# Optimization experiments

Measured on AMD Instinct MI355X. Metric: run time of the kernel, lower is better.

Reference implementation:

```python
import jax, jax.numpy as jnp
import numpy as np

N = 20000      # atoms
E = 320000     # edges
F = 128        # node_size (hard-pinned by split(128) / expand to 384)
RBF = 20
RC = 5.0
ITERS = 3
NM = 64        # molecules in batch


def setup_inputs() -> dict:
    key = jax.random.key(0)
    ks = iter(jax.random.split(key, 64))
    def nrm(shape, scale=0.05):
        return jax.random.normal(next(ks), shape, dtype=jnp.float32) * scale
    inp = {}
    inp["z"] = jax.random.randint(next(ks), (N,), 0, 119)
    inp["graph"] = jax.random.randint(next(ks), (E, 2), 0, N)
    inp["edges_dist"] = jax.random.uniform(next(ks), (E,), minval=0.5, maxval=RC, dtype=jnp.float32)
    sense = jax.random.normal(next(ks), (E, 3), dtype=jnp.float32)
    inp["edges_sense"] = sense / jnp.linalg.norm(sense, axis=1, keepdims=True)
    inp["graph_idx"] = jnp.sort(jax.random.randint(next(ks), (N,), 0, NM))
    # parameters (stacked over ITERS message/update blocks)
    inp["emb"] = nrm((119, F), 1.0)
    inp["mw1"] = nrm((ITERS, F, F)); inp["mb1"] = nrm((ITERS, F))
    inp["mw2"] = nrm((ITERS, 3 * F, F)); inp["mb2"] = nrm((ITERS, 3 * F))
    inp["ew"] = nrm((ITERS, 3 * F, RBF)); inp["eb"] = nrm((ITERS, 3 * F))
    inp["uw"] = nrm((ITERS, F, F)); inp["vw"] = nrm((ITERS, F, F))
    inp["aw1"] = nrm((ITERS, F, 2 * F)); inp["ab1"] = nrm((ITERS, F))
    inp["aw2"] = nrm((ITERS, 3 * F, F)); inp["ab2"] = nrm((ITERS, 3 * F))
    inp["ow1"] = nrm((F, F)); inp["ob1"] = nrm((F,))
    inp["ow2"] = nrm((1, F)); inp["ob2"] = nrm((1,))
    return inp


def reference(z, graph, edges_dist, edges_sense, graph_idx,
              emb, mw1, mb1, mw2, mb2, ew, eb,
              uw, vw, aw1, ab1, aw2, ab2, ow1, ob1, ow2, ob2):
    src = graph[:, 0]   # scatter target (index_add index)
    dst = graph[:, 1]   # gather source (neighbour)
    s = emb[z]                                  # [N, F]
    v = jnp.zeros((N, 3, F), dtype=s.dtype)     # [N, 3, F]
    # edge-level precompute (same every iteration)
    n = jnp.arange(1, RBF + 1, dtype=jnp.float32)
    d = edges_dist[:, None]
    rbf = jnp.sin(n * jnp.pi * d / RC) / d                              # [E, RBF]
    cut = 0.5 * (jnp.cos(jnp.pi * edges_dist / RC) + 1.0) * (edges_dist < RC)  # [E]
    for i in range(ITERS):
        # --- Message block ---
        a = jax.nn.silu(s @ mw1[i].T + mb1[i]) @ mw2[i].T + mb2[i]      # [N, 3F]
        dist_rep = (rbf @ ew[i].T + eb[i]) * cut[:, None]               # [E, 3F]
        res = a[dst] * dist_rep                                         # [E, 3F]
        rv, rs, rd = res[:, :F], res[:, F:2 * F], res[:, 2 * F:]
        resv = v[dst] * rv[:, None, :] + edges_sense[:, :, None] * rd[:, None, :]  # [E,3,F]
        s = s + 2.0 * jax.ops.segment_sum(rs, src, num_segments=N)
        v = v + 2.0 * jax.ops.segment_sum(resv, src, num_segments=N)
        # --- Update block ---
        Uv = v @ uw[i].T                                                # [N,3,F]
        Vv = v @ vw[i].T
        h = jnp.concatenate([s, jnp.linalg.norm(Vv, axis=1)], axis=-1)  # [N, 2F]
        a2 = jax.nn.silu(h @ aw1[i].T + ab1[i]) @ aw2[i].T + ab2[i]     # [N, 3F]
        avv, asv, ass = a2[:, :F], a2[:, F:2 * F], a2[:, 2 * F:]
        s = s + ass + asv * jnp.sum(Uv * Vv, axis=1)
        v = v + avv[:, None, :] * Uv
    out = jax.nn.silu(s @ ow1.T + ob1) @ ow2.T + ob2                    # [N, 1]
    return jax.ops.segment_sum(out, graph_idx, num_segments=NM)         # [NM, 1]
```

## Files before the change

### kernel.cpp

```cpp
#include <hip/hip_runtime.h>
#include <math.h>

#define NN 20000
#define NE 320000
#define FD 128
#define RBFN 20
#define RC_ 5.0f
#define NITER 3
#define NMOL 64
#define F3 384
#define F2 256
#define PI_ 3.14159265358979323846f
#define KB 128
#define LPAD 8

typedef __attribute__((ext_vector_type(8))) short  bf16x8;
typedef __attribute__((ext_vector_type(4))) float  floatx4;
typedef unsigned short u16;

__device__ __forceinline__ u16 f2b(float x) {
    union { float f; unsigned int u; } v; v.f = x;
    unsigned int u = v.u;
    return (u16)((u + 0x7fffu + ((u >> 16) & 1u)) >> 16);
}
__device__ __forceinline__ float b2f(u16 x) {
    union { unsigned int u; float f; } v; v.u = ((unsigned int)x) << 16;
    return v.f;
}

__global__ __launch_bounds__(256) void cvt_w_kernel(
    const float* s0, int n0, const float* s1, int n1, const float* s2, int n2,
    const float* s3, int n3, const float* s4, int n4, const float* s5, int n5,
    const float* s6, int n6, u16* __restrict__ dst)
{
    int idx = blockIdx.x * 256 + threadIdx.x;
    if (idx < n0) { dst[idx] = f2b(s0[idx]); return; } idx -= n0; dst += n0;
    if (idx < n1) { dst[idx] = f2b(s1[idx]); return; } idx -= n1; dst += n1;
    if (idx < n2) { dst[idx] = f2b(s2[idx]); return; } idx -= n2; dst += n2;
    if (idx < n3) { dst[idx] = f2b(s3[idx]); return; } idx -= n3; dst += n3;
    if (idx < n4) { dst[idx] = f2b(s4[idx]); return; } idx -= n4; dst += n4;
    if (idx < n5) { dst[idx] = f2b(s5[idx]); return; } idx -= n5; dst += n5;
    if (idx < n6) { dst[idx] = f2b(s6[idx]); }
}

__global__ __launch_bounds__(256) void cvt_ew_kernel(const float* __restrict__ ew,
    u16* __restrict__ ewb)
{
    int idx = blockIdx.x * 256 + threadIdx.x;
    if (idx >= NITER * F3 * 32) return;
    int k = idx & 31;
    int row = idx >> 5;
    ewb[idx] = (k < RBFN) ? f2b(ew[row * RBFN + k]) : (u16)0;
}

__global__ __launch_bounds__(256) void embed_kernel(const int* __restrict__ z,
    const float* __restrict__ emb, float* __restrict__ s, u16* __restrict__ sbf)
{
    int idx = blockIdx.x * 256 + threadIdx.x;
    if (idx >= NN * FD) return;
    int n = idx >> 7, f = idx & 127;
    float v = emb[z[n] * FD + f];
    s[idx] = v; sbf[idx] = f2b(v);
}

__global__ __launch_bounds__(256) void zero_f_kernel(float* __restrict__ p, int n)
{
    int idx = blockIdx.x * 256 + threadIdx.x;
    if (idx < n) p[idx] = 0.f;
}

__global__ __launch_bounds__(256) void zero_i_kernel(int* __restrict__ p, int n)
{
    int idx = blockIdx.x * 256 + threadIdx.x;
    if (idx < n) p[idx] = 0;
}

__global__ __launch_bounds__(256) void csr_count_kernel(const int* __restrict__ graph,
    int* __restrict__ cnt)
{
    int e = blockIdx.x * 256 + threadIdx.x;
    if (e >= NE) return;
    atomicAdd(&cnt[graph[2 * e]], 1);
}

__global__ __launch_bounds__(1024) void csr_scan_kernel(const int* __restrict__ cnt,
    int* __restrict__ row_ptr, int* __restrict__ cursor)
{
    __shared__ int sd[1024];
    int tid = threadIdx.x;
    const int chunk = (NN + 1023) / 1024;
    int start = tid * chunk;
    int end = start + chunk; if (end > NN) end = NN;
    int sum = 0;
    for (int j = start; j < end; j++) sum += cnt[j];
    sd[tid] = sum;
    __syncthreads();
    for (int off = 1; off < 1024; off <<= 1) {
        int v = 0;
        if (tid >= off) v = sd[tid - off];
        __syncthreads();
        if (tid >= off) sd[tid] += v;
        __syncthreads();
    }
    int run = (tid == 0) ? 0 : sd[tid - 1];
    for (int j = start; j < end; j++) {
        row_ptr[j] = run;
        cursor[j]  = run;
        run += cnt[j];
    }
    if (tid == 0) row_ptr[NN] = NE;
}

__global__ __launch_bounds__(256) void csr_scatter_kernel(const int* __restrict__ graph,
    int* __restrict__ cursor, int* __restrict__ edge_list)
{
    int e = blockIdx.x * 256 + threadIdx.x;
    if (e >= NE) return;
    int p = atomicAdd(&cursor[graph[2 * e]], 1);
    edge_list[p] = e;
}

__global__ __launch_bounds__(256) void edge_stream_kernel(
    const int* __restrict__ edge_list, const int* __restrict__ graph,
    const float* __restrict__ dist, const float* __restrict__ sense,
    u16* __restrict__ rbf_bf, float* __restrict__ cut_p,
    float* __restrict__ sense_p, int* __restrict__ dst_p)
{
    int j = blockIdx.x * 256 + threadIdx.x;
    if (j >= NE) return;
    int e = edge_list[j];
    float d = dist[e];
    float inv = 1.f / d;
    float base = PI_ * d / RC_;
    u16* rb = rbf_bf + (size_t)j * 32;
    #pragma unroll
    for (int k = 0; k < RBFN; k++)
        rb[k] = f2b(sinf((float)(k + 1) * base) * inv);
    #pragma unroll
    for (int k = RBFN; k < 32; k++) rb[k] = 0;
    cut_p[j] = 0.5f * (cosf(base) + 1.f) * (d < RC_ ? 1.f : 0.f);
    dst_p[j] = graph[2 * e + 1];
    sense_p[3 * j + 0] = sense[3 * e + 0];
    sense_p[3 * j + 1] = sense[3 * e + 1];
    sense_p[3 * j + 2] = sense[3 * e + 2];
}

template<bool SILU>
__global__ __launch_bounds__(256) void gemm_bf16(const u16* __restrict__ A,
    const u16* __restrict__ Wt, const float* __restrict__ bias,
    float* __restrict__ C, u16* __restrict__ Cb, int M, int K, int Nc)
{
    __shared__ u16 As[64][KB + LPAD];
    __shared__ u16 Bs[64][KB + LPAD];
    const int bm = blockIdx.x * 64;
    const int bn = blockIdx.y * 64;
    const int tid = threadIdx.x;
    const int r = tid >> 2;
    const int q = tid & 3;
    const int wave = tid >> 6;
    const int lane = tid & 63;
    const int wm = (wave >> 1) * 32;
    const int wn = (wave & 1) * 32;
    const int quad = lane >> 4;
    const int lr = lane & 15;

    floatx4 acc[2][2];
    #pragma unroll
    for (int i = 0; i < 2; i++)
        #pragma unroll
        for (int j = 0; j < 2; j++)
            acc[i][j] = (floatx4)0.f;

    for (int ko = 0; ko < K; ko += KB) {
        {
            int gm = bm + r;
            u16* dA = &As[r][q * 32];
            if (gm < M) {
                const u16* ap = A + (size_t)gm * K + ko + q * 32;
                #pragma unroll
                for (int x = 0; x < 32; x += 8)
                    *(bf16x8*)&dA[x] = *(const bf16x8*)(ap + x);
            } else {
                #pragma unroll
                for (int x = 0; x < 32; x += 8)
                    *(bf16x8*)&dA[x] = (bf16x8)0;
            }
        }
        {
            int gn = bn + r;
            const u16* wp = Wt + (size_t)gn * K + ko + q * 32;
            u16* dB = &Bs[r][q * 32];
            #pragma unroll
            for (int x = 0; x < 32; x += 8)
                *(bf16x8*)&dB[x] = *(const bf16x8*)(wp + x);
        }
        __syncthreads();
        #pragma unroll
        for (int kk = 0; kk < KB; kk += 32) {
            bf16x8 a0 = *(const bf16x8*)&As[wm + lr     ][kk + quad * 8];
            bf16x8 a1 = *(const bf16x8*)&As[wm + 16 + lr][kk + quad * 8];
            bf16x8 b0 = *(const bf16x8*)&Bs[wn + lr     ][kk + quad * 8];
            bf16x8 b1 = *(const bf16x8*)&Bs[wn + 16 + lr][kk + quad * 8];
            acc[0][0] = __builtin_amdgcn_mfma_f32_16x16x32_bf16(a0, b0, acc[0][0], 0, 0, 0);
            acc[0][1] = __builtin_amdgcn_mfma_f32_16x16x32_bf16(a0, b1, acc[0][1], 0, 0, 0);
            acc[1][0] = __builtin_amdgcn_mfma_f32_16x16x32_bf16(a1, b0, acc[1][0], 0, 0, 0);
            acc[1][1] = __builtin_amdgcn_mfma_f32_16x16x32_bf16(a1, b1, acc[1][1], 0, 0, 0);
        }
        __syncthreads();
    }

    #pragma unroll
    for (int i = 0; i < 2; i++) {
        #pragma unroll
        for (int j = 0; j < 2; j++) {
            int gn = bn + wn + j * 16 + lr;
            float bb = bias ? bias[gn] : 0.f;
            #pragma unroll
            for (int rr = 0; rr < 4; rr++) {
                int gm = bm + wm + i * 16 + quad * 4 + rr;
                if (gm < M) {
                    float v = acc[i][j][rr] + bb;
                    if (SILU) v = v / (1.f + __expf(-v));
                    if (C)  C [(size_t)gm * Nc + gn] = v;
                    if (Cb) Cb[(size_t)gm * Nc + gn] = f2b(v);
                }
            }
        }
    }
}

template<int K1>
__global__ __launch_bounds__(256) void mlp_kernel(const u16* __restrict__ A,
    const u16* __restrict__ W1, const float* __restrict__ b1,
    const u16* __restrict__ W2, const float* __restrict__ b2,
    u16* __restrict__ Ob, int M)
{
    __shared__ u16 As[64][KB + LPAD];
    __shared__ u16 Ws[128][KB + LPAD];
    __shared__ u16 T[64][KB + LPAD];
    const int bm = blockIdx.x * 64;
    const int tid = threadIdx.x;
    const int wave = tid >> 6, lane = tid & 63;
    const int wm  = (wave >> 1) * 32;
    const int wn1 = (wave & 1) * 64;
    const int wn  = (wave & 1) * 32;
    const int quad = lane >> 4, lr = lane & 15;
    const int r = tid >> 2, q = tid & 3;

    floatx4 acc1[2][4];
    #pragma unroll
    for (int i = 0; i < 2; i++)
        #pragma unroll
        for (int j = 0; j < 4; j++) acc1[i][j] = (floatx4)0.f;

    for (int ko = 0; ko < K1; ko += KB) {
        {
            int gm = bm + r;
            u16* dA = &As[r][q * 32];
            if (gm < M) {
                const u16* ap = A + (size_t)gm * K1 + ko + q * 32;
                #pragma unroll
                for (int x = 0; x < 32; x += 8)
                    *(bf16x8*)&dA[x] = *(const bf16x8*)(ap + x);
            } else {
                #pragma unroll
                for (int x = 0; x < 32; x += 8)
                    *(bf16x8*)&dA[x] = (bf16x8)0;
            }
            #pragma unroll
            for (int h = 0; h < 2; h++) {
                int wr = r + h * 64;
                const u16* wp = W1 + (size_t)wr * K1 + ko + q * 32;
                u16* dW = &Ws[wr][q * 32];
                #pragma unroll
                for (int x = 0; x < 32; x += 8)
                    *(bf16x8*)&dW[x] = *(const bf16x8*)(wp + x);
            }
        }
        __syncthreads();
        #pragma unroll
        for (int kk = 0; kk < KB; kk += 32) {
            bf16x8 a0 = *(const bf16x8*)&As[wm + lr     ][kk + quad * 8];
            bf16x8 a1 = *(const bf16x8*)&As[wm + 16 + lr][kk + quad * 8];
            #pragma unroll
            for (int j = 0; j < 4; j++) {
                bf16x8 b = *(const bf16x8*)&Ws[wn1 + j * 16 + lr][kk + quad * 8];
                acc1[0][j] = __builtin_amdgcn_mfma_f32_16x16x32_bf16(a0, b, acc1[0][j], 0, 0, 0);
                acc1[1][j] = __builtin_amdgcn_mfma_f32_16x16x32_bf16(a1, b, acc1[1][j], 0, 0, 0);
            }
        }
        __syncthreads();
    }
    #pragma unroll
    for (int i = 0; i < 2; i++) {
        #pragma unroll
        for (int j = 0; j < 4; j++) {
            int col = wn1 + j * 16 + lr;
            float bb = b1[col];
            #pragma unroll
            for (int rr = 0; rr < 4; rr++) {
                int row = wm + i * 16 + quad * 4 + rr;
                float v = acc1[i][j][rr] + bb;
                v = v / (1.f + __expf(-v));
                T[row][col] = f2b(v);
            }
        }
    }
    __syncthreads();

    for (int c0 = 0; c0 < F3; c0 += 64) {
        {
            const u16* wp = W2 + (size_t)(c0 + r) * KB + q * 32;
            u16* dW = &Ws[r][q * 32];
            #pragma unroll
            for (int x = 0; x < 32; x += 8)
                *(bf16x8*)&dW[x] = *(const bf16x8*)(wp + x);
        }
        __syncthreads();
        floatx4 acc2[2][2];
        #pragma unroll
        for (int i = 0; i < 2; i++)
            #pragma unroll
            for (int j = 0; j < 2; j++) acc2[i][j] = (floatx4)0.f;
        #pragma unroll
        for (int kk = 0; kk < KB; kk += 32) {
            bf16x8 a0 = *(const bf16x8*)&T[wm + lr     ][kk + quad * 8];
            bf16x8 a1 = *(const bf16x8*)&T[wm + 16 + lr][kk + quad * 8];
            bf16x8 b0 = *(const bf16x8*)&Ws[wn + lr     ][kk + quad * 8];
            bf16x8 b1 = *(const bf16x8*)&Ws[wn + 16 + lr][kk + quad * 8];
            acc2[0][0] = __builtin_amdgcn_mfma_f32_16x16x32_bf16(a0, b0, acc2[0][0], 0, 0, 0);
            acc2[0][1] = __builtin_amdgcn_mfma_f32_16x16x32_bf16(a0, b1, acc2[0][1], 0, 0, 0);
            acc2[1][0] = __builtin_amdgcn_mfma_f32_16x16x32_bf16(a1, b0, acc2[1][0], 0, 0, 0);
            acc2[1][1] = __builtin_amdgcn_mfma_f32_16x16x32_bf16(a1, b1, acc2[1][1], 0, 0, 0);
        }
        #pragma unroll
        for (int i = 0; i < 2; i++) {
            #pragma unroll
            for (int j = 0; j < 2; j++) {
                int gn = c0 + wn + j * 16 + lr;
                float bb = b2[gn];
                #pragma unroll
                for (int rr = 0; rr < 4; rr++) {
                    int gm = bm + wm + i * 16 + quad * 4 + rr;
                    if (gm < M)
                        Ob[(size_t)gm * F3 + gn] = f2b(acc2[i][j][rr] + bb);
                }
            }
        }
        __syncthreads();
    }
}

__global__ __launch_bounds__(256) void gemm_uv(const u16* __restrict__ A,
    const u16* __restrict__ Wu, const u16* __restrict__ Wv,
    u16* __restrict__ U, u16* __restrict__ V, int M)
{
    __shared__ u16 As[64][KB + LPAD];
    __shared__ u16 Bu[64][KB + LPAD];
    __shared__ u16 Bv[64][KB + LPAD];
    const int bm = blockIdx.x * 64;
    const int bn = blockIdx.y * 64;
    const int tid = threadIdx.x;
    const int r = tid >> 2;
    const int q = tid & 3;
    const int wave = tid >> 6;
    const int lane = tid & 63;
    const int wm = (wave >> 1) * 32;
    const int wn = (wave & 1) * 32;
    const int quad = lane >> 4;
    const int lr = lane & 15;

    floatx4 au[2][2], av[2][2];
    #pragma unroll
    for (int i = 0; i < 2; i++)
        #pragma unroll
        for (int j = 0; j < 2; j++) { au[i][j] = (floatx4)0.f; av[i][j] = (floatx4)0.f; }

    {
        int gm = bm + r;
        u16* dA = &As[r][q * 32];
        if (gm < M) {
            const u16* ap = A + (size_t)gm * KB + q * 32;
            #pragma unroll
            for (int x = 0; x < 32; x += 8)
                *(bf16x8*)&dA[x] = *(const bf16x8*)(ap + x);
        } else {
            #pragma unroll
            for (int x = 0; x < 32; x += 8)
                *(bf16x8*)&dA[x] = (bf16x8)0;
        }
        int gn = bn + r;
        const u16* up = Wu + (size_t)gn * KB + q * 32;
        const u16* vp = Wv + (size_t)gn * KB + q * 32;
        u16* dU = &Bu[r][q * 32];
        u16* dV = &Bv[r][q * 32];
        #pragma unroll
        for (int x = 0; x < 32; x += 8) {
            *(bf16x8*)&dU[x] = *(const bf16x8*)(up + x);
            *(bf16x8*)&dV[x] = *(const bf16x8*)(vp + x);
        }
    }
    __syncthreads();
    #pragma unroll
    for (int kk = 0; kk < KB; kk += 32) {
        bf16x8 a0 = *(const bf16x8*)&As[wm + lr     ][kk + quad * 8];
        bf16x8 a1 = *(const bf16x8*)&As[wm + 16 + lr][kk + quad * 8];
        bf16x8 u0 = *(const bf16x8*)&Bu[wn + lr     ][kk + quad * 8];
        bf16x8 u1 = *(const bf16x8*)&Bu[wn + 16 + lr][kk + quad * 8];
        bf16x8 v0 = *(const bf16x8*)&Bv[wn + lr     ][kk + quad * 8];
        bf16x8 v1 = *(const bf16x8*)&Bv[wn + 16 + lr][kk + quad * 8];
        au[0][0] = __builtin_amdgcn_mfma_f32_16x16x32_bf16(a0, u0, au[0][0], 0, 0, 0);
        au[0][1] = __builtin_amdgcn_mfma_f32_16x16x32_bf16(a0, u1, au[0][1], 0, 0, 0);
        au[1][0] = __builtin_amdgcn_mfma_f32_16x16x32_bf16(a1, u0, au[1][0], 0, 0, 0);
        au[1][1] = __builtin_amdgcn_mfma_f32_16x16x32_bf16(a1, u1, au[1][1], 0, 0, 0);
        av[0][0] = __builtin_amdgcn_mfma_f32_16x16x32_bf16(a0, v0, av[0][0], 0, 0, 0);
        av[0][1] = __builtin_amdgcn_mfma_f32_16x16x32_bf16(a0, v1, av[0][1], 0, 0, 0);
        av[1][0] = __builtin_amdgcn_mfma_f32_16x16x32_bf16(a1, v0, av[1][0], 0, 0, 0);
        av[1][1] = __builtin_amdgcn_mfma_f32_16x16x32_bf16(a1, v1, av[1][1], 0, 0, 0);
    }
    #pragma unroll
    for (int i = 0; i < 2; i++) {
        #pragma unroll
        for (int j = 0; j < 2; j++) {
            int gn = bn + wn + j * 16 + lr;
            #pragma unroll
            for (int rr = 0; rr < 4; rr++) {
                int gm = bm + wm + i * 16 + quad * 4 + rr;
                if (gm < M) {
                    U[(size_t)gm * FD + gn] = f2b(au[i][j][rr]);
                    V[(size_t)gm * FD + gn] = f2b(av[i][j][rr]);
                }
            }
        }
    }
}

__global__ __launch_bounds__(256) void edge_mfma_kernel(
    const u16* __restrict__ rbf_bf, const float* __restrict__ cut_p,
    const float* __restrict__ sense_p, const int* __restrict__ dst_p,
    const u16* __restrict__ ewb, const float* __restrict__ eb,
    const u16* __restrict__ a_bf, const float* __restrict__ s_in,
    const float* __restrict__ v_in, const u16* __restrict__ v_bf,
    const int* __restrict__ row_ptr,
    float* __restrict__ s_out, u16* __restrict__ s_obf,
    float* __restrict__ v_out, u16* __restrict__ v_obf)
{
    __shared__ float sdrep[16][F3 + 4];
    __shared__ float scut[16];
    __shared__ float ssen[48];
    __shared__ int   sdst[16];
    __shared__ float red[4 * 128];

    const int n = blockIdx.x;
    const int tid = threadIdx.x;
    const int wave = tid >> 6;
    const int lane = tid & 63;
    const int quad = lane >> 4;
    const int lr = lane & 15;
    const int f = tid & 127;
    const int half = tid >> 7;

    int beg = row_ptr[n], end = row_ptr[n + 1];
    float accs = 0.f, accv0 = 0.f, accv1 = 0.f, accv2 = 0.f;

    for (int t0 = beg; t0 < end; t0 += 16) {
        int cnt = end - t0; if (cnt > 16) cnt = 16;
        __syncthreads();
        if (tid < 16) {
            scut[tid] = (tid < cnt) ? cut_p[t0 + tid] : 0.f;
            sdst[tid] = (tid < cnt) ? dst_p[t0 + tid] : 0;
        }
        if (tid >= 64 && tid < 64 + 3 * cnt) ssen[tid - 64] = sense_p[3 * t0 + (tid - 64)];
        bf16x8 afrag;
        int ge = t0 + lr;
        if (ge < end) afrag = *(const bf16x8*)&rbf_bf[(size_t)ge * 32 + quad * 8];
        else          afrag = (bf16x8)0;
        floatx4 dacc[6];
        #pragma unroll
        for (int nt = 0; nt < 6; nt++) {
            int nrow = (wave * 6 + nt) * 16 + lr;
            bf16x8 bfrag = *(const bf16x8*)&ewb[(size_t)nrow * 32 + quad * 8];
            dacc[nt] = __builtin_amdgcn_mfma_f32_16x16x32_bf16(afrag, bfrag, (floatx4)0.f, 0, 0, 0);
        }
        __syncthreads();
        #pragma unroll
        for (int nt = 0; nt < 6; nt++) {
            int ncol = (wave * 6 + nt) * 16 + lr;
            float ebn = eb[ncol];
            #pragma unroll
            for (int rr = 0; rr < 4; rr++) {
                int e = quad * 4 + rr;
                sdrep[e][ncol] = (dacc[nt][rr] + ebn) * scut[e];
            }
        }
        __syncthreads();
        int e0 = half * 8;
        int e1 = e0 + 8; if (e1 > cnt) e1 = cnt;
        for (int e = e0; e < e1; e++) {
            int dst = sdst[e];
            float drv = sdrep[e][f];
            float drs = sdrep[e][FD + f];
            float drd = sdrep[e][2 * FD + f];
            const u16* ar = a_bf + (size_t)dst * F3;
            float rv = b2f(ar[f])          * drv;
            float rs = b2f(ar[FD + f])     * drs;
            float rd = b2f(ar[2 * FD + f]) * drd;
            accs += rs;
            const u16* vr = v_bf + (size_t)dst * F3;
            float sx = ssen[3 * e], sy = ssen[3 * e + 1], sz = ssen[3 * e + 2];
            accv0 += b2f(vr[f])          * rv + sx * rd;
            accv1 += b2f(vr[FD + f])     * rv + sy * rd;
            accv2 += b2f(vr[2 * FD + f]) * rv + sz * rd;
        }
    }
    __syncthreads();
    if (half == 1) {
        red[f] = accs; red[128 + f] = accv0; red[256 + f] = accv1; red[384 + f] = accv2;
    }
    __syncthreads();
    if (half == 0) {
        accs  += red[f];       accv0 += red[128 + f];
        accv1 += red[256 + f]; accv2 += red[384 + f];
        int nb = n * FD + f;
        float so = s_in[nb] + 2.f * accs;
        s_out[nb] = so; s_obf[nb] = f2b(so);
        int vb = n * F3 + f;
        float w0 = v_in[vb]           + 2.f * accv0;
        float w1 = v_in[vb + FD]      + 2.f * accv1;
        float w2 = v_in[vb + 2 * FD]  + 2.f * accv2;
        v_out[vb]          = w0; v_obf[vb]          = f2b(w0);
        v_out[vb + FD]     = w1; v_obf[vb + FD]     = f2b(w1);
        v_out[vb + 2 * FD] = w2; v_obf[vb + 2 * FD] = f2b(w2);
    }
}

__global__ __launch_bounds__(256) void build_h_kernel(const u16* __restrict__ sbf,
    const u16* __restrict__ Vv, u16* __restrict__ h)
{
    int idx = blockIdx.x * 256 + threadIdx.x;
    if (idx >= NN * FD) return;
    int n = idx >> 7, f = idx & 127;
    h[n * F2 + f] = sbf[idx];
    float x0 = b2f(Vv[n * F3 + f]);
    float x1 = b2f(Vv[n * F3 + FD + f]);
    float x2 = b2f(Vv[n * F3 + 2 * FD + f]);
    h[n * F2 + FD + f] = f2b(sqrtf(x0 * x0 + x1 * x1 + x2 * x2));
}

__global__ __launch_bounds__(256) void update_kernel(const float* __restrict__ s_mid,
    const float* __restrict__ v_mid, const u16* __restrict__ a2,
    const u16* __restrict__ Uv, const u16* __restrict__ Vv,
    float* __restrict__ s_out, u16* __restrict__ s_obf,
    float* __restrict__ v_out, u16* __restrict__ v_obf)
{
    int idx = blockIdx.x * 256 + threadIdx.x;
    if (idx >= NN * FD) return;
    int n = idx >> 7, f = idx & 127;
    int vb = n * F3 + f;
    float u0 = b2f(Uv[vb]), u1 = b2f(Uv[vb + FD]), u2 = b2f(Uv[vb + 2 * FD]);
    float w0 = b2f(Vv[vb]), w1 = b2f(Vv[vb + FD]), w2 = b2f(Vv[vb + 2 * FD]);
    float dot = u0 * w0 + u1 * w1 + u2 * w2;
    float avv = b2f(a2[n * F3 + f]);
    float asv = b2f(a2[n * F3 + FD + f]);
    float ass = b2f(a2[n * F3 + 2 * FD + f]);
    float so = s_mid[idx] + ass + asv * dot;
    s_out[idx] = so; s_obf[idx] = f2b(so);
    float y0 = v_mid[vb]          + avv * u0;
    float y1 = v_mid[vb + FD]     + avv * u1;
    float y2 = v_mid[vb + 2 * FD] + avv * u2;
    v_out[vb]          = y0; v_obf[vb]          = f2b(y0);
    v_out[vb + FD]     = y1; v_obf[vb + FD]     = f2b(y1);
    v_out[vb + 2 * FD] = y2; v_obf[vb + 2 * FD] = f2b(y2);
}

__global__ __launch_bounds__(256) void node_out_kernel(const float* __restrict__ t,
    const float* __restrict__ ow2, const float* __restrict__ ob2,
    float* __restrict__ nodeval)
{
    int gt = blockIdx.x * 256 + threadIdx.x;
    int n = gt >> 6;
    int lane = threadIdx.x & 63;
    if (n >= NN) return;
    float v = t[n * FD + lane] * ow2[lane] + t[n * FD + 64 + lane] * ow2[64 + lane];
    #pragma unroll
    for (int off = 32; off > 0; off >>= 1) v += __shfl_down(v, off);
    if (lane == 0) nodeval[n] = v + ob2[0];
}

__global__ __launch_bounds__(1024) void mol_reduce_kernel(const float* __restrict__ nodeval,
    const int* __restrict__ gidx, float* __restrict__ out)
{
    __shared__ float mol[NMOL];
    int tid = threadIdx.x;
    if (tid < NMOL) mol[tid] = 0.f;
    __syncthreads();
    int cur = -1; float acc = 0.f;
    for (int x = tid; x < NN; x += 1024) {
        int g = gidx[x];
        float v = nodeval[x];
        if (g != cur) {
            if (cur >= 0) atomicAdd(&mol[cur], acc);
            cur = g; acc = v;
        } else acc += v;
    }
    if (cur >= 0) atomicAdd(&mol[cur], acc);
    __syncthreads();
    if (tid < NMOL) out[tid] = mol[tid];
}

extern "C" void kernel_launch(void* const* d_in, const int* in_sizes, int n_in,
                              void* d_out, int out_size, void* d_ws, size_t ws_size,
                              hipStream_t stream)
{
    const int*   z     = (const int*)d_in[0];
    const int*   graph = (const int*)d_in[1];
    const float* dist  = (const float*)d_in[2];
    const float* sense = (const float*)d_in[3];
    const int*   gidx  = (const int*)d_in[4];
    const float* emb   = (const float*)d_in[5];
    const float* mw1   = (const float*)d_in[6];
    const float* mb1   = (const float*)d_in[7];
    const float* mw2   = (const float*)d_in[8];
    const float* mb2   = (const float*)d_in[9];
    const float* ew    = (const float*)d_in[10];
    const float* eb    = (const float*)d_in[11];
    const float* uw    = (const float*)d_in[12];
    const float* vw    = (const float*)d_in[13];
    const float* aw1   = (const float*)d_in[14];
    const float* ab1   = (const float*)d_in[15];
    const float* aw2   = (const float*)d_in[16];
    const float* ab2   = (const float*)d_in[17];
    const float* ow1   = (const float*)d_in[18];
    const float* ob1   = (const float*)d_in[19];
    const float* ow2   = (const float*)d_in[20];
    const float* ob2   = (const float*)d_in[21];
    float* out = (float*)d_out;

    float* W = (float*)d_ws;
    float* s_a    = W; W += (size_t)NN * FD;
    float* s_b    = W; W += (size_t)NN * FD;
    float* v_a    = W; W += (size_t)NN * F3;
    float* v_b    = W; W += (size_t)NN * F3;
    float* cut_p  = W; W += (size_t)NE;
    float* sns_p  = W; W += (size_t)NE * 3;
    float* tfin   = W; W += (size_t)NN * FD;
    float* nodeval= W; W += (size_t)NN;
    u16* U = (u16*)W;
    u16* sbf_a = U; U += (size_t)NN * FD;
    u16* sbf_b = U; U += (size_t)NN * FD;
    u16* vbf_a = U; U += (size_t)NN * F3;
    u16* vbf_b = U; U += (size_t)NN * F3;
    u16* a_bf  = U; U += (size_t)NN * F3;
    u16* a2_bf = U; U += (size_t)NN * F3;
    u16* Uv_bf = U; U += (size_t)NN * F3;
    u16* Vv_bf = U; U += (size_t)NN * F3;
    u16* rbf_bf= U; U += (size_t)NE * 32;
    u16* ewb   = U; U += (size_t)NITER * F3 * 32;
    u16* wb    = U; U += 557056;
    int* ip = (int*)U;
    int* row_ptr   = ip; ip += NN + 1;
    int* cnt       = ip; ip += NN;
    int* cursor    = ip; ip += NN;
    int* edge_list = ip; ip += NE;
    int* dst_p     = ip; ip += NE;
    u16* h_bf = a_bf;

    u16* wb_mw1 = wb;
    u16* wb_mw2 = wb + 49152;
    u16* wb_uw  = wb + 196608;
    u16* wb_vw  = wb + 245760;
    u16* wb_aw1 = wb + 294912;
    u16* wb_aw2 = wb + 393216;
    u16* wb_ow1 = wb + 540672;
    const int WTOT = 557056;

    const int TB = 256;
    dim3 b256(TB);

    cvt_w_kernel<<<dim3((WTOT + TB - 1) / TB), b256, 0, stream>>>(
        mw1, 49152, mw2, 147456, uw, 49152, vw, 49152, aw1, 98304, aw2, 147456,
        ow1, 16384, wb);
    cvt_ew_kernel<<<dim3((NITER * F3 * 32 + TB - 1) / TB), b256, 0, stream>>>(ew, ewb);
    embed_kernel<<<dim3((NN * FD + TB - 1) / TB), b256, 0, stream>>>(z, emb, s_a, sbf_a);
    zero_f_kernel<<<dim3((NN * F3 + TB - 1) / TB), b256, 0, stream>>>(v_a, NN * F3);
    zero_i_kernel<<<dim3((NN * F3 / 2 + TB - 1) / TB), b256, 0, stream>>>((int*)vbf_a, NN * F3 / 2);
    zero_i_kernel<<<dim3((NN + TB - 1) / TB), b256, 0, stream>>>(cnt, NN);
    csr_count_kernel<<<dim3((NE + TB - 1) / TB), b256, 0, stream>>>(graph, cnt);
    csr_scan_kernel<<<dim3(1), dim3(1024), 0, stream>>>(cnt, row_ptr, cursor);
    csr_scatter_kernel<<<dim3((NE + TB - 1) / TB), b256, 0, stream>>>(graph, cursor, edge_list);
    edge_stream_kernel<<<dim3((NE + TB - 1) / TB), b256, 0, stream>>>(
        edge_list, graph, dist, sense, rbf_bf, cut_p, sns_p, dst_p);

    dim3 gM((NN + 63) / 64);
    dim3 gN2((NN + 63) / 64, FD / 64);
    dim3 gV2((3 * NN + 63) / 64, FD / 64);

    for (int i = 0; i < NITER; i++) {
        mlp_kernel<128><<<gM, b256, 0, stream>>>(sbf_a,
            wb_mw1 + (size_t)i * FD * FD, mb1 + (size_t)i * FD,
            wb_mw2 + (size_t)i * F3 * FD, mb2 + (size_t)i * F3, a_bf, NN);
        edge_mfma_kernel<<<dim3(NN), b256, 0, stream>>>(
            rbf_bf, cut_p, sns_p, dst_p,
            ewb + (size_t)i * F3 * 32, eb + (size_t)i * F3,
            a_bf, s_a, v_a, vbf_a, row_ptr, s_b, sbf_b, v_b, vbf_b);
        gemm_uv<<<gV2, b256, 0, stream>>>(vbf_b, wb_uw + (size_t)i * FD * FD,
            wb_vw + (size_t)i * FD * FD, Uv_bf, Vv_bf, 3 * NN);
        build_h_kernel<<<dim3((NN * FD + TB - 1) / TB), b256, 0, stream>>>(sbf_b, Vv_bf, h_bf);
        mlp_kernel<256><<<gM, b256, 0, stream>>>(h_bf,
            wb_aw1 + (size_t)i * FD * F2, ab1 + (size_t)i * FD,
            wb_aw2 + (size_t)i * F3 * FD, ab2 + (size_t)i * F3, a2_bf, NN);
        update_kernel<<<dim3((NN * FD + TB - 1) / TB), b256, 0, stream>>>(
            s_b, v_b, a2_bf, Uv_bf, Vv_bf, s_a, sbf_a, v_a, vbf_a);
    }

    gemm_bf16<true><<<gN2, b256, 0, stream>>>(sbf_a, wb_ow1, ob1, tfin, nullptr, NN, FD, FD);
    node_out_kernel<<<dim3((NN * 64 + TB - 1) / TB), b256, 0, stream>>>(tfin, ow2, ob2, nodeval);
    mol_reduce_kernel<<<dim3(1), dim3(1024), 0, stream>>>(nodeval, gidx, out);
}
```

Before: 971.3 us.

## Pack gathered node features per channel for coalesced 8-byte edge gathers

The message MLP output and the bf16 copy of v are now written in a packed [node][feature][4] layout, so the edge kernel fetches the three channel values of a neighbour with one ushort4 load instead of three strided scalar loads. The per-edge distance representation in shared memory is also stored as packed bf16 in the same interleaved layout. The aim is fewer gather transactions and less LDS traffic in the dominant edge kernel. In exchange the gathered buffers grow by a third because of the padding lane, and storing the distance representation in bf16 instead of fp32 lowers its precision.

Result: slower. 996.8 us (+2.6%).

```diff
diff --git a/kernel.cpp b/kernel.cpp
--- a/kernel.cpp
+++ b/kernel.cpp
@@ -13,6 +13,7 @@
 #define PI_ 3.14159265358979323846f
 #define KB 128
 #define LPAD 8
+#define SD_STRIDE 516
 
 typedef __attribute__((ext_vector_type(8))) short  bf16x8;
 typedef __attribute__((ext_vector_type(4))) float  floatx4;
@@ -148,7 +149,7 @@
 template<bool SILU>
 __global__ __launch_bounds__(256) void gemm_bf16(const u16* __restrict__ A,
     const u16* __restrict__ Wt, const float* __restrict__ bias,
-    float* __restrict__ C, u16* __restrict__ Cb, int M, int K, int Nc)
+    float* __restrict__ C, int M, int K, int Nc)
 {
     __shared__ u16 As[64][KB + LPAD];
     __shared__ u16 Bs[64][KB + LPAD];
@@ -221,15 +222,14 @@
                 if (gm < M) {
                     float v = acc[i][j][rr] + bb;
                     if (SILU) v = v / (1.f + __expf(-v));
-                    if (C)  C [(size_t)gm * Nc + gn] = v;
-                    if (Cb) Cb[(size_t)gm * Nc + gn] = f2b(v);
+                    C[(size_t)gm * Nc + gn] = v;
                 }
             }
         }
     }
 }
 
-template<int K1>
+template<int K1, bool PACK>
 __global__ __launch_bounds__(256) void mlp_kernel(const u16* __restrict__ A,
     const u16* __restrict__ W1, const float* __restrict__ b1,
     const u16* __restrict__ W2, const float* __restrict__ b2,
@@ -342,8 +342,13 @@
                 #pragma unroll
                 for (int rr = 0; rr < 4; rr++) {
                     int gm = bm + wm + i * 16 + quad * 4 + rr;
-                    if (gm < M)
-                        Ob[(size_t)gm * F3 + gn] = f2b(acc2[i][j][rr] + bb);
+                    if (gm < M) {
+                        u16 val = f2b(acc2[i][j][rr] + bb);
+                        if (PACK)
+                            Ob[(size_t)gm * 512 + (gn & 127) * 4 + (gn >> 7)] = val;
+                        else
+                            Ob[(size_t)gm * F3 + gn] = val;
+                    }
                 }
             }
         }
@@ -439,15 +444,15 @@
     const u16* __restrict__ rbf_bf, const float* __restrict__ cut_p,
     const float* __restrict__ sense_p, const int* __restrict__ dst_p,
     const u16* __restrict__ ewb, const float* __restrict__ eb,
-    const u16* __restrict__ a_bf, const float* __restrict__ s_in,
-    const float* __restrict__ v_in, const u16* __restrict__ v_bf,
+    const u16* __restrict__ a_pk, const float* __restrict__ s_in,
+    const float* __restrict__ v_in, const u16* __restrict__ v_pk,
     const int* __restrict__ row_ptr,
     float* __restrict__ s_out, u16* __restrict__ s_obf,
     float* __restrict__ v_out, u16* __restrict__ v_obf)
 {
-    __shared__ float sdrep[16][F3 + 4];
+    __shared__ u16   sdrep[16 * SD_STRIDE];
     __shared__ float scut[16];
-    __shared__ float ssen[48];
+    __shared__ float ssen[16][4];
     __shared__ int   sdst[16];
     __shared__ float red[4 * 128];
 
@@ -470,7 +475,10 @@
             scut[tid] = (tid < cnt) ? cut_p[t0 + tid] : 0.f;
             sdst[tid] = (tid < cnt) ? dst_p[t0 + tid] : 0;
         }
-        if (tid >= 64 && tid < 64 + 3 * cnt) ssen[tid - 64] = sense_p[3 * t0 + (tid - 64)];
+        if (tid >= 64 && tid < 64 + 3 * cnt) {
+            int x = tid - 64;
+            ssen[x / 3][x % 3] = sense_p[3 * t0 + x];
+        }
         bf16x8 afrag;
         int ge = t0 + lr;
         if (ge < end) afrag = *(const bf16x8*)&rbf_bf[(size_t)ge * 32 + quad * 8];
@@ -486,31 +494,30 @@
         #pragma unroll
         for (int nt = 0; nt < 6; nt++) {
             int ncol = (wave * 6 + nt) * 16 + lr;
+            int fc = ncol & 127, c = ncol >> 7;
             float ebn = eb[ncol];
             #pragma unroll
             for (int rr = 0; rr < 4; rr++) {
                 int e = quad * 4 + rr;
-                sdrep[e][ncol] = (dacc[nt][rr] + ebn) * scut[e];
-            }
-        }
-        __syncthreads();
-        int e0 = half * 8;
-        int e1 = e0 + 8; if (e1 > cnt) e1 = cnt;
-        for (int e = e0; e < e1; e++) {
+                sdrep[e * SD_STRIDE + fc * 4 + c] = f2b((dacc[nt][rr] + ebn) * scut[e]);
+            }
+        }
+        __syncthreads();
+        int nh = cnt - half * 8; if (nh > 8) nh = 8;
+        for (int k = 0; k < nh; k++) {
+            int e = half * 8 + k;
             int dst = sdst[e];
-            float drv = sdrep[e][f];
-            float drs = sdrep[e][FD + f];
-            float drd = sdrep[e][2 * FD + f];
-            const u16* ar = a_bf + (size_t)dst * F3;
-            float rv = b2f(ar[f])          * drv;
-            float rs = b2f(ar[FD + f])     * drs;
-            float rd = b2f(ar[2 * FD + f]) * drd;
+            ushort4 dr = *(const ushort4*)&sdrep[e * SD_STRIDE + f * 4];
+            float drv = b2f(dr.x), drs = b2f(dr.y), drd = b2f(dr.z);
+            ushort4 a4 = *(const ushort4*)(a_pk + (size_t)dst * 512 + f * 4);
+            float rv = b2f(a4.x) * drv;
+            float rs = b2f(a4.y) * drs;
+            float rd = b2f(a4.z) * drd;
             accs += rs;
-            const u16* vr = v_bf + (size_t)dst * F3;
-            float sx = ssen[3 * e], sy = ssen[3 * e + 1], sz = ssen[3 * e + 2];
-            accv0 += b2f(vr[f])          * rv + sx * rd;
-            accv1 += b2f(vr[FD + f])     * rv + sy * rd;
-            accv2 += b2f(vr[2 * FD + f]) * rv + sz * rd;
+            ushort4 v4 = *(const ushort4*)(v_pk + (size_t)dst * 512 + f * 4);
+            accv0 += b2f(v4.x) * rv + ssen[e][0] * rd;
+            accv1 += b2f(v4.y) * rv + ssen[e][1] * rd;
+            accv2 += b2f(v4.z) * rv + ssen[e][2] * rd;
         }
     }
     __syncthreads();
@@ -551,7 +558,7 @@
     const float* __restrict__ v_mid, const u16* __restrict__ a2,
     const u16* __restrict__ Uv, const u16* __restrict__ Vv,
     float* __restrict__ s_out, u16* __restrict__ s_obf,
-    float* __restrict__ v_out, u16* __restrict__ v_obf)
+    float* __restrict__ v_out, u16* __restrict__ v_pk)
 {
     int idx = blockIdx.x * 256 + threadIdx.x;
     if (idx >= NN * FD) return;
@@ -568,9 +575,11 @@
     float y0 = v_mid[vb]          + avv * u0;
     float y1 = v_mid[vb + FD]     + avv * u1;
     float y2 = v_mid[vb + 2 * FD] + avv * u2;
-    v_out[vb]          = y0; v_obf[vb]          = f2b(y0);
-    v_out[vb + FD]     = y1; v_obf[vb + FD]     = f2b(y1);
-    v_out[vb + 2 * FD] = y2; v_obf[vb + 2 * FD] = f2b(y2);
+    v_out[vb]          = y0;
+    v_out[vb + FD]     = y1;
+    v_out[vb + 2 * FD] = y2;
+    ushort4 pk; pk.x = f2b(y0); pk.y = f2b(y1); pk.z = f2b(y2); pk.w = 0;
+    *(ushort4*)(v_pk + (size_t)idx * 4) = pk;
 }
 
 __global__ __launch_bounds__(256) void node_out_kernel(const float* __restrict__ t,
@@ -643,14 +652,14 @@
     float* v_b    = W; W += (size_t)NN * F3;
     float* cut_p  = W; W += (size_t)NE;
     float* sns_p  = W; W += (size_t)NE * 3;
-    float* tfin   = W; W += (size_t)NN * FD;
     float* nodeval= W; W += (size_t)NN;
     u16* U = (u16*)W;
     u16* sbf_a = U; U += (size_t)NN * FD;
     u16* sbf_b = U; U += (size_t)NN * FD;
-    u16* vbf_a = U; U += (size_t)NN * F3;
     u16* vbf_b = U; U += (size_t)NN * F3;
-    u16* a_bf  = U; U += (size_t)NN * F3;
+    u16* a_pk  = U; U += (size_t)NN * 512;
+    u16* v_pk  = U; U += (size_t)NN * 512;
+    u16* h_bf  = U; U += (size_t)NN * F2;
     u16* a2_bf = U; U += (size_t)NN * F3;
     u16* Uv_bf = U; U += (size_t)NN * F3;
     u16* Vv_bf = U; U += (size_t)NN * F3;
@@ -663,7 +672,7 @@
     int* cursor    = ip; ip += NN;
     int* edge_list = ip; ip += NE;
     int* dst_p     = ip; ip += NE;
-    u16* h_bf = a_bf;
+    float* tfin = s_b;
 
     u16* wb_mw1 = wb;
     u16* wb_mw2 = wb + 49152;
@@ -683,7 +692,7 @@
     cvt_ew_kernel<<<dim3((NITER * F3 * 32 + TB - 1) / TB), b256, 0, stream>>>(ew, ewb);
     embed_kernel<<<dim3((NN * FD + TB - 1) / TB), b256, 0, stream>>>(z, emb, s_a, sbf_a);
     zero_f_kernel<<<dim3((NN * F3 + TB - 1) / TB), b256, 0, stream>>>(v_a, NN * F3);
-    zero_i_kernel<<<dim3((NN * F3 / 2 + TB - 1) / TB), b256, 0, stream>>>((int*)vbf_a, NN * F3 / 2);
+    zero_i_kernel<<<dim3((NN * 256 + TB - 1) / TB), b256, 0, stream>>>((int*)v_pk, NN * 256);
     zero_i_kernel<<<dim3((NN + TB - 1) / TB), b256, 0, stream>>>(cnt, NN);
     csr_count_kernel<<<dim3((NE + TB - 1) / TB), b256, 0, stream>>>(graph, cnt);
     csr_scan_kernel<<<dim3(1), dim3(1024), 0, stream>>>(cnt, row_ptr, cursor);
@@ -696,24 +705,24 @@
     dim3 gV2((3 * NN + 63) / 64, FD / 64);
 
     for (int i = 0; i < NITER; i++) {
-        mlp_kernel<128><<<gM, b256, 0, stream>>>(sbf_a,
+        mlp_kernel<128, true><<<gM, b256, 0, stream>>>(sbf_a,
             wb_mw1 + (size_t)i * FD * FD, mb1 + (size_t)i * FD,
-            wb_mw2 + (size_t)i * F3 * FD, mb2 + (size_t)i * F3, a_bf, NN);
+            wb_mw2 + (size_t)i * F3 * FD, mb2 + (size_t)i * F3, a_pk, NN);
         edge_mfma_kernel<<<dim3(NN), b256, 0, stream>>>(
             rbf_bf, cut_p, sns_p, dst_p,
             ewb + (size_t)i * F3 * 32, eb + (size_t)i * F3,
-            a_bf, s_a, v_a, vbf_a, row_ptr, s_b, sbf_b, v_b, vbf_b);
+            a_pk, s_a, v_a, v_pk, row_ptr, s_b, sbf_b, v_b, vbf_b);
         gemm_uv<<<gV2, b256, 0, stream>>>(vbf_b, wb_uw + (size_t)i * FD * FD,
             wb_vw + (size_t)i * FD * FD, Uv_bf, Vv_bf, 3 * NN);
         build_h_kernel<<<dim3((NN * FD + TB - 1) / TB), b256, 0, stream>>>(sbf_b, Vv_bf, h_bf);
-        mlp_kernel<256><<<gM, b256, 0, stream>>>(h_bf,
+        mlp_kernel<256, false><<<gM, b256, 0, stream>>>(h_bf,
             wb_aw1 + (size_t)i * FD * F2, ab1 + (size_t)i * FD,
             wb_aw2 + (size_t)i * F3 * FD, ab2 + (size_t)i * F3, a2_bf, NN);
         update_kernel<<<dim3((NN * FD + TB - 1) / TB), b256, 0, stream>>>(
-            s_b, v_b, a2_bf, Uv_bf, Vv_bf, s_a, sbf_a, v_a, vbf_a);
-    }
-
-    gemm_bf16<true><<<gN2, b256, 0, stream>>>(sbf_a, wb_ow1, ob1, tfin, nullptr, NN, FD, FD);
+            s_b, v_b, a2_bf, Uv_bf, Vv_bf, s_a, sbf_a, v_a, v_pk);
+    }
+
+    gemm_bf16<true><<<gN2, b256, 0, stream>>>(sbf_a, wb_ow1, ob1, tfin, NN, FD, FD);
     node_out_kernel<<<dim3((NN * 64 + TB - 1) / TB), b256, 0, stream>>>(tfin, ow2, ob2, nodeval);
     mol_reduce_kernel<<<dim3(1), dim3(1024), 0, stream>>>(nodeval, gidx, out);
 }
```
